# Kernel tuning notes

Measured on AMD Instinct MI355X. Metric: run time of the kernel, lower is better.

## Reference

```python
import jax, jax.numpy as jnp
import numpy as np

B, N, D = 2, 8192, 1024
H, Dh = 16, 64
P = H * Dh
EPS = 1e-6
DECAY_BIAS_SHIFT = 2.0


def setup_inputs() -> dict:
    key = jax.random.key(0)
    ks = jax.random.split(key, 7)
    s_in = 1.0 / np.sqrt(D)
    s_out = 1.0 / np.sqrt(P)
    return {
        "x": jax.random.normal(ks[0], (B, N, D), jnp.float32),
        "Wq": jax.random.normal(ks[1], (D, P), jnp.float32) * s_in,
        "Wk": jax.random.normal(ks[2], (D, P), jnp.float32) * s_in,
        "Wv": jax.random.normal(ks[3], (D, P), jnp.float32) * s_in,
        "Wo": jax.random.normal(ks[4], (P, D), jnp.float32) * s_out,
        "Wa": jax.random.normal(ks[5], (D, H), jnp.float32) * s_in,
        "ba": jnp.zeros((H,), jnp.float32),
    }


def _elu_plus_one(x):
    return jax.nn.elu(x) + 1.0


def _ssd_scan(q, k, v, a, eps):
    # q,k,v: (B,H,N,Dh); a: (B,H,N) in (0,1)
    # Recurrence: S_t = a_t*S_{t-1} + k_t v_t^T ; z_t = a_t*z_{t-1} + k_t
    # out_t = (q_t @ S_t) / (q_t . z_t + eps)
    qT = jnp.moveaxis(q, 2, 0)  # (N,B,H,Dh)
    kT = jnp.moveaxis(k, 2, 0)
    vT = jnp.moveaxis(v, 2, 0)
    aT = jnp.moveaxis(a, 2, 0)  # (N,B,H)

    Bb, Hh, _, Dk = q.shape
    Dv = v.shape[-1]
    S0 = jnp.zeros((Bb, Hh, Dk, Dv), q.dtype)
    z0 = jnp.zeros((Bb, Hh, Dk), q.dtype)

    def step(carry, inp):
        S, z = carry
        qt, kt, vt, at = inp
        S = at[..., None, None] * S + kt[..., :, None] * vt[..., None, :]
        z = at[..., None] * z + kt
        num = jnp.einsum("bhk,bhkv->bhv", qt, S)
        den = jnp.einsum("bhk,bhk->bh", qt, z) + eps
        return (S, z), num / den[..., None]

    _, outT = jax.lax.scan(step, (S0, z0), (qT, kT, vT, aT))
    return jnp.moveaxis(outT, 0, 2)  # (B,H,N,Dv)


def reference(x, Wq, Wk, Wv, Wo, Wa, ba):
    b, n, _ = x.shape
    q = (x @ Wq).reshape(b, n, H, Dh).transpose(0, 2, 1, 3)
    k = (x @ Wk).reshape(b, n, H, Dh).transpose(0, 2, 1, 3)
    v = (x @ Wv).reshape(b, n, H, Dh).transpose(0, 2, 1, 3)
    q = _elu_plus_one(q)
    k = _elu_plus_one(k)
    a = jax.nn.sigmoid(x @ Wa + ba + DECAY_BIAS_SHIFT)  # (B,N,H)
    a = a.transpose(0, 2, 1)  # (B,H,N)
    out = _ssd_scan(q, k, v, a, EPS)  # (B,H,N,Dh)
    out = out.transpose(0, 2, 1, 3).reshape(b, n, P)
    return out @ Wo
```

## Files before the change

kernel.cpp:

```cpp
#include <hip/hip_runtime.h>
#include <stdint.h>

#define HH 16
#define DH 64
#define DD 1024
#define PP 1024
#define NNLEN 8192
#define BBATCH 2
#define MM (BBATCH*NNLEN)
#define CCHUNK 128
#define LCH 64
#define NGRP 16
#define GCH 8
#define EPSV 1e-6f

typedef unsigned short u16;
typedef __attribute__((ext_vector_type(4))) unsigned short u16x4;
typedef __attribute__((ext_vector_type(8))) unsigned short u16x8;
typedef __attribute__((ext_vector_type(8))) __bf16 bf16x8;
typedef __attribute__((ext_vector_type(4))) float f32x4;

__device__ __forceinline__ u16 f2bf(float f) {
  unsigned x = __float_as_uint(f);
  return (u16)((x + 0x7fffu + ((x >> 16) & 1u)) >> 16);
}
__device__ __forceinline__ float bf2f(u16 u) {
  return __uint_as_float(((unsigned)u) << 16);
}

__device__ __forceinline__ void gl2lds16(const void* g, void* l) {
  __builtin_amdgcn_global_load_lds(
      reinterpret_cast<__attribute__((address_space(1))) void*>(
          reinterpret_cast<uintptr_t>(g)),
      reinterpret_cast<__attribute__((address_space(3))) void*>(
          reinterpret_cast<uintptr_t>(l)),
      16, 0, 0);
}

__device__ __forceinline__ bf16x8 ldsw(const u16* base, int row, int col) {
  union { u16x8 u; bf16x8 b; } cv;
  cv.u = *(const u16x8*)&base[row * 64 + (col ^ ((row & 7) << 3))];
  return cv.b;
}

__global__ __launch_bounds__(256)
void prep_all(const float* __restrict__ x, u16* __restrict__ xb,
              const float* __restrict__ Wq, u16* __restrict__ WqT,
              const float* __restrict__ Wk, u16* __restrict__ WkT,
              const float* __restrict__ Wv, u16* __restrict__ WvT,
              const float* __restrict__ Wo, u16* __restrict__ WoT,
              const float* __restrict__ Wa, u16* __restrict__ WaT) {
  __shared__ float tile[32][33];
  const int bid = blockIdx.x;
  const int tid = threadIdx.x;
  if (bid < 8192) {
    size_t i = ((size_t)bid * 256 + tid) * 8;
    f32x4 a = *(const f32x4*)(x + i);
    f32x4 b = *(const f32x4*)(x + i + 4);
    u16x8 o;
    o[0] = f2bf(a[0]); o[1] = f2bf(a[1]); o[2] = f2bf(a[2]); o[3] = f2bf(a[3]);
    o[4] = f2bf(b[0]); o[5] = f2bf(b[1]); o[6] = f2bf(b[2]); o[7] = f2bf(b[3]);
    *(u16x8*)(xb + i) = o;
    return;
  }
  if (bid < 12288) {
    const int t = (bid - 8192) >> 10;
    const int sub = (bid - 8192) & 1023;
    const float* in = (t == 0) ? Wq : (t == 1) ? Wk : (t == 2) ? Wv : Wo;
    u16* out = (t == 0) ? WqT : (t == 1) ? WkT : (t == 2) ? WvT : WoT;
    const int bx = (sub & 31) * 32, by = (sub >> 5) * 32;
    const int tx = tid & 31, ty = tid >> 5;
    for (int i2 = ty; i2 < 32; i2 += 8)
      tile[i2][tx] = in[(size_t)(by + i2) * 1024 + bx + tx];
    __syncthreads();
    for (int i2 = ty; i2 < 32; i2 += 8)
      out[(size_t)(bx + i2) * 1024 + by + tx] = f2bf(tile[tx][i2]);
    return;
  }
  {
    int idx = (bid - 12288) * 256 + tid;
    WaT[idx] = f2bf(Wa[(idx & 1023) * 16 + (idx >> 10)]);
  }
}

__global__ __launch_bounds__(256)
void a_proj(const u16* __restrict__ xb, const u16* __restrict__ WaT,
            const float* __restrict__ ba, float* __restrict__ abuf) {
  __shared__ __align__(16) u16 As[256 * 32];
  __shared__ __align__(16) u16 Bs[16 * 32];
  const int tid = threadIdx.x;
  const int brow = blockIdx.x * 256;
  const int l = tid & 63, wid = tid >> 6;
  const int la = l & 15, kb8 = (l >> 4) * 8;
  const int sr = tid >> 2, se = (tid & 3) * 8;

  f32x4 acc[4];
#pragma unroll
  for (int mi = 0; mi < 4; ++mi) acc[mi] = (f32x4){0.f, 0.f, 0.f, 0.f};

  for (int kt = 0; kt < 32; ++kt) {
    const int k0 = kt * 32;
    __syncthreads();
#pragma unroll
    for (int i = 0; i < 4; ++i)
      gl2lds16(xb + (size_t)(brow + i * 64 + sr) * DD + k0 + se,
               &As[i * 2048 + wid * 512]);
    if (wid == 0)
      gl2lds16(WaT + (size_t)(l >> 2) * DD + k0 + (l & 3) * 8, &Bs[0]);
    __syncthreads();
    union { u16x8 u; bf16x8 b; } cvb;
    cvb.u = *(const u16x8*)&Bs[la * 32 + kb8];
#pragma unroll
    for (int mi = 0; mi < 4; ++mi) {
      union { u16x8 u; bf16x8 b; } cva;
      cva.u = *(const u16x8*)&As[(wid * 64 + mi * 16 + la) * 32 + kb8];
      acc[mi] = __builtin_amdgcn_mfma_f32_16x16x32_bf16(cva.b, cvb.b, acc[mi], 0, 0, 0);
    }
  }
  const float bav = ba[la];
#pragma unroll
  for (int mi = 0; mi < 4; ++mi)
#pragma unroll
    for (int rr = 0; rr < 4; ++rr) {
      int row = brow + wid * 64 + mi * 16 + ((l >> 4) << 2) + rr;
      float t = acc[mi][rr] + bav + 2.0f;
      abuf[(size_t)row * HH + la] = 1.f / (1.f + __expf(-t));
    }
}

template<int NCT>
__global__ __launch_bounds__(1024, 4)
void gemm16(const u16* __restrict__ A, const u16* __restrict__ Bt,
            void* __restrict__ Cout) {
  __shared__ __align__(16) u16 As[2][256 * 64];
  __shared__ __align__(16) u16 Bs[2][256 * 64];
  const int tid = threadIdx.x;
  const int nwg = gridDim.x;
  const int f = blockIdx.x;
  const int swz = (f & 7) * (nwg >> 3) + (f >> 3);
  const int brow = (swz / NCT) * 256;
  const int bcol = (swz % NCT) * 256;
  const int l = tid & 63;
  const int wid = tid >> 6;
  const int wr = wid >> 2;
  const int wc = wid & 3;
  const int la = l & 15, kb8 = (l >> 4) * 8;
  const int K = 1024;
  const int srow = l >> 3;
  const int scol = ((l & 7) * 8) ^ (srow << 3);
  const int ldso = (wid * 2) * 512;

  f32x4 acc[4][4];
#pragma unroll
  for (int i = 0; i < 4; ++i)
#pragma unroll
    for (int j = 0; j < 4; ++j) acc[i][j] = (f32x4){0.f, 0.f, 0.f, 0.f};

#pragma unroll
  for (int j = 0; j < 2; ++j) {
    const int r0 = (wid * 2 + j) * 8 + srow;
    gl2lds16(A  + (size_t)(brow + r0) * K + scol, &As[0][ldso + j * 512]);
    gl2lds16(Bt + (size_t)(bcol + r0) * K + scol, &Bs[0][ldso + j * 512]);
  }
  asm volatile("s_waitcnt vmcnt(0)" ::: "memory");
  __builtin_amdgcn_s_barrier();

  const int NKT = K / 64;
  for (int kt = 0; kt < NKT; ++kt) {
    const u16* lA = As[kt & 1];
    const u16* lB = Bs[kt & 1];
    u16* nA = As[(kt + 1) & 1];
    u16* nB = Bs[(kt + 1) & 1];
    const int knext = (kt + 1) * 64;
    const bool more = (kt + 1 < NKT);

    if (more) {
#pragma unroll
      for (int j = 0; j < 2; ++j) {
        const int r0 = (wid * 2 + j) * 8 + srow;
        gl2lds16(A  + (size_t)(brow + r0) * K + knext + scol,
                 nA + ldso + j * 512);
        gl2lds16(Bt + (size_t)(bcol + r0) * K + knext + scol,
                 nB + ldso + j * 512);
      }
    }

    bf16x8 bfr[4][2];
#pragma unroll
    for (int n2 = 0; n2 < 4; ++n2)
#pragma unroll
      for (int kk = 0; kk < 2; ++kk)
        bfr[n2][kk] = ldsw(lB, wc * 64 + n2 * 16 + la, kk * 32 + kb8);

#pragma unroll
    for (int m2 = 0; m2 < 4; ++m2) {
      bf16x8 af0 = ldsw(lA, wr * 64 + m2 * 16 + la, kb8);
      bf16x8 af1 = ldsw(lA, wr * 64 + m2 * 16 + la, 32 + kb8);
      __builtin_amdgcn_s_setprio(1);
#pragma unroll
      for (int n2 = 0; n2 < 4; ++n2) {
        acc[m2][n2] = __builtin_amdgcn_mfma_f32_16x16x32_bf16(
            af0, bfr[n2][0], acc[m2][n2], 0, 0, 0);
        acc[m2][n2] = __builtin_amdgcn_mfma_f32_16x16x32_bf16(
            af1, bfr[n2][1], acc[m2][n2], 0, 0, 0);
      }
      __builtin_amdgcn_s_setprio(0);
    }

    if (more) {
      asm volatile("s_waitcnt vmcnt(0)" ::: "memory");
      __builtin_amdgcn_s_barrier();
    }
  }

  const int wrow = wr * 64, wcol = wc * 64;
  u16* base = (u16*)Cout + (size_t)(bcol >> 10) * ((size_t)MM * 1024);
  const bool act = (bcol < 2048);
#pragma unroll
  for (int mi = 0; mi < 4; ++mi)
#pragma unroll
    for (int ni = 0; ni < 4; ++ni)
#pragma unroll
      for (int rr = 0; rr < 4; ++rr) {
        int row = brow + wrow + mi * 16 + ((l >> 4) << 2) + rr;
        int c2 = (bcol & 1023) + wcol + ni * 16 + la;
        float v = acc[mi][ni][rr];
        if (act) v = v > 0.f ? v + 1.f : __expf(v);
        base[(size_t)row * 1024 + c2] = f2bf(v);
      }
}

template<int NCT>
__global__ __launch_bounds__(512)
void gemm_db(const u16* __restrict__ A, const u16* __restrict__ Bt,
             float* __restrict__ Cout) {
  __shared__ __align__(16) u16 As[2][256 * 64];
  __shared__ __align__(16) u16 Bs[2][256 * 64];
  const int tid = threadIdx.x;
  const int nwg = gridDim.x;
  const int f = blockIdx.x;
  const int swz = (f & 7) * (nwg >> 3) + (f >> 3);
  const int brow = (swz / NCT) * 256;
  const int bcol = (swz % NCT) * 256;
  const int l = tid & 63;
  const int wid = tid >> 6;
  const int wr = wid >> 2;
  const int wc = wid & 3;
  const int la = l & 15, kb8 = (l >> 4) * 8;
  const int K = 1024;
  const int srow = l >> 3;
  const int scol = ((l & 7) * 8) ^ (srow << 3);
  const int ldso = (wid * 2) * 512;

  f32x4 acc[8][4];
#pragma unroll
  for (int i = 0; i < 8; ++i)
#pragma unroll
    for (int j = 0; j < 4; ++j) acc[i][j] = (f32x4){0.f, 0.f, 0.f, 0.f};

#pragma unroll
  for (int h = 0; h < 2; ++h)
#pragma unroll
    for (int j = 0; j < 2; ++j) {
      const int r0 = h * 128 + (wid * 2 + j) * 8 + srow;
      gl2lds16(A  + (size_t)(brow + r0) * K + scol, &As[0][h * 8192 + ldso + j * 512]);
      gl2lds16(Bt + (size_t)(bcol + r0) * K + scol, &Bs[0][h * 8192 + ldso + j * 512]);
    }
  asm volatile("s_waitcnt vmcnt(0)" ::: "memory");
  __builtin_amdgcn_s_barrier();

  const int NKT = K / 64;
  for (int kt = 0; kt < NKT; ++kt) {
    const u16* lA = As[kt & 1];
    const u16* lB = Bs[kt & 1];
    u16* nA = As[(kt + 1) & 1];
    u16* nB = Bs[(kt + 1) & 1];
    const int knext = (kt + 1) * 64;
    const bool more = (kt + 1 < NKT);

    if (more) {
#pragma unroll
      for (int h = 0; h < 2; ++h)
#pragma unroll
        for (int j = 0; j < 2; ++j) {
          const int r0 = h * 128 + (wid * 2 + j) * 8 + srow;
          gl2lds16(A  + (size_t)(brow + r0) * K + knext + scol,
                   nA + h * 8192 + ldso + j * 512);
          gl2lds16(Bt + (size_t)(bcol + r0) * K + knext + scol,
                   nB + h * 8192 + ldso + j * 512);
        }
    }

    bf16x8 af[4][2], bfr[4][2];
#pragma unroll
    for (int m2 = 0; m2 < 4; ++m2)
#pragma unroll
      for (int kk = 0; kk < 2; ++kk)
        af[m2][kk] = ldsw(lA, wr * 128 + m2 * 16 + la, kk * 32 + kb8);
#pragma unroll
    for (int n2 = 0; n2 < 4; ++n2)
#pragma unroll
      for (int kk = 0; kk < 2; ++kk)
        bfr[n2][kk] = ldsw(lB, wc * 64 + n2 * 16 + la, kk * 32 + kb8);

    __builtin_amdgcn_s_setprio(1);
#pragma unroll
    for (int m2 = 0; m2 < 4; ++m2)
#pragma unroll
      for (int n2 = 0; n2 < 4; ++n2)
#pragma unroll
        for (int kk = 0; kk < 2; ++kk)
          acc[m2][n2] = __builtin_amdgcn_mfma_f32_16x16x32_bf16(
              af[m2][kk], bfr[n2][kk], acc[m2][n2], 0, 0, 0);
    __builtin_amdgcn_s_setprio(0);

#pragma unroll
    for (int m2 = 0; m2 < 4; ++m2)
#pragma unroll
      for (int kk = 0; kk < 2; ++kk)
        af[m2][kk] = ldsw(lA, wr * 128 + 64 + m2 * 16 + la, kk * 32 + kb8);

    __builtin_amdgcn_s_setprio(1);
#pragma unroll
    for (int m2 = 0; m2 < 4; ++m2)
#pragma unroll
      for (int n2 = 0; n2 < 4; ++n2)
#pragma unroll
        for (int kk = 0; kk < 2; ++kk)
          acc[4 + m2][n2] = __builtin_amdgcn_mfma_f32_16x16x32_bf16(
              af[m2][kk], bfr[n2][kk], acc[4 + m2][n2], 0, 0, 0);
    __builtin_amdgcn_s_setprio(0);

    if (more) {
      asm volatile("s_waitcnt vmcnt(0)" ::: "memory");
      __builtin_amdgcn_s_barrier();
    }
  }

  const int wrow = wr * 128, wcol = wc * 64;
#pragma unroll
  for (int mi = 0; mi < 8; ++mi)
#pragma unroll
    for (int ni = 0; ni < 4; ++ni)
#pragma unroll
      for (int rr = 0; rr < 4; ++rr) {
        int row = brow + wrow + mi * 16 + ((l >> 4) << 2) + rr;
        int col = bcol + wcol + ni * 16 + la;
        Cout[(size_t)row * 1024 + col] = acc[mi][ni][rr];
      }
}

__global__ __launch_bounds__(256)
void chunk_local_scan(const u16* __restrict__ kb, const u16* __restrict__ vb,
                      const float* __restrict__ abuf,
                      u16* __restrict__ Sbuf, float* __restrict__ zbuf,
                      float* __restrict__ cAbuf,
                      float* __restrict__ GAgg, float* __restrict__ zGAgg,
                      float* __restrict__ dpbuf) {
  const int g = blockIdx.x & (NGRP - 1);
  const int bh = blockIdx.x >> 4;
  const int h = bh & (HH - 1);
  const int b = bh >> 4;
  __shared__ __align__(16) u16 KT[64 * 64];
  __shared__ __align__(16) u16 VTl[64 * 64];
  __shared__ float wshA[GCH][64];
  __shared__ float dchA[GCH];
  const int tid = threadIdx.x;
  const int r = tid >> 2, e = (tid & 3) * 16;
  const int l = tid & 63, w = tid >> 6;
  const int kb8 = (l >> 4) << 3, la = l & 15;
  const int dw = 16 * w + ((l >> 4) << 2);
  const int dkz = tid >> 2, tqz = (tid & 3) * 16, swkz = (dkz & 7) << 3;
  const int c0 = g * GCH;
  const int rowbase0 = b * NNLEN + c0 * LCH;

#pragma unroll
  for (int ii = 0; ii < 2; ++ii) {
    const int i = w * 2 + ii;
    const int blkc = bh * CCHUNK + c0 + i;
    float v = __logf(abuf[(size_t)(rowbase0 + i * LCH + l) * HH + h]);
#pragma unroll
    for (int d = 1; d < 64; d <<= 1) {
      float u = __shfl_up(v, d);
      if (l >= d) v += u;
    }
    cAbuf[(size_t)blkc * 64 + l] = v;
    float tot = __shfl(v, 63);
    wshA[i][l] = __expf(tot - v);
    if (l == 0) dchA[i] = __expf(tot);
  }
  __syncthreads();
  if (tid == 0) {
    float rp = 1.f;
#pragma unroll
    for (int i = 0; i < GCH; ++i) {
      dpbuf[bh * CCHUNK + c0 + i] = rp;
      rp *= dchA[i];
    }
  }

  f32x4 run[4];
#pragma unroll
  for (int ni = 0; ni < 4; ++ni) run[ni] = (f32x4){0.f, 0.f, 0.f, 0.f};
  float zrun = 0.f;

  const u16* kp = kb + (size_t)(rowbase0 + r) * PP + h * DH + e;
  const u16* vp = vb + (size_t)(rowbase0 + r) * PP + h * DH + e;
  u16x8 k0 = *(const u16x8*)kp, k1 = *(const u16x8*)(kp + 8);
  u16x8 v0 = *(const u16x8*)vp, v1 = *(const u16x8*)(vp + 8);

  for (int i = 0; i < GCH; ++i) {
    const int blkc = bh * CCHUNK + c0 + i;
    if (i) __syncthreads();

    {
      const float wt = wshA[i][r];
#pragma unroll
      for (int j = 0; j < 8; ++j) {
        int d0 = e + j, d1 = e + 8 + j;
        KT[d0 * 64 + (r ^ ((d0 & 7) << 3))] = f2bf(bf2f(k0[j]) * wt);
        KT[d1 * 64 + (r ^ ((d1 & 7) << 3))] = f2bf(bf2f(k1[j]) * wt);
        VTl[d0 * 64 + (r ^ ((d0 & 7) << 3))] = v0[j];
        VTl[d1 * 64 + (r ^ ((d1 & 7) << 3))] = v1[j];
      }
    }
    __syncthreads();

    if (i + 1 < GCH) {
      const int rb = rowbase0 + (i + 1) * LCH;
      kp = kb + (size_t)(rb + r) * PP + h * DH + e;
      vp = vb + (size_t)(rb + r) * PP + h * DH + e;
      k0 = *(const u16x8*)kp; k1 = *(const u16x8*)(kp + 8);
      v0 = *(const u16x8*)vp; v1 = *(const u16x8*)(vp + 8);
    }

    const float dch = dchA[i];
    f32x4 s[4];
#pragma unroll
    for (int ni = 0; ni < 4; ++ni) s[ni] = (f32x4){0.f, 0.f, 0.f, 0.f};
#pragma unroll
    for (int kk = 0; kk < 2; ++kk) {
      bf16x8 av = ldsw(VTl, 16 * w + la, kk * 32 + kb8);
#pragma unroll
      for (int ni = 0; ni < 4; ++ni)
        s[ni] = __builtin_amdgcn_mfma_f32_16x16x32_bf16(
            av, ldsw(KT, 16 * ni + la, kk * 32 + kb8), s[ni], 0, 0, 0);
    }

    u16* Sc = Sbuf + (size_t)blkc * 4096;
#pragma unroll
    for (int ni = 0; ni < 4; ++ni)
#pragma unroll
      for (int rr = 0; rr < 4; ++rr)
        Sc[(dw + rr) * 64 + 16 * ni + la] = f2bf(run[ni][rr]);
#pragma unroll
    for (int ni = 0; ni < 4; ++ni)
#pragma unroll
      for (int rr = 0; rr < 4; ++rr)
        run[ni][rr] = dch * run[ni][rr] + s[ni][rr];

    {
      float zp = 0.f;
#pragma unroll
      for (int i2 = 0; i2 < 16; ++i2)
        zp += bf2f(KT[dkz * 64 + ((tqz + i2) ^ swkz)]);
      zp += __shfl_xor(zp, 1);
      zp += __shfl_xor(zp, 2);
      if ((tid & 3) == 0) zbuf[(size_t)blkc * 64 + dkz] = zrun;
      zrun = dch * zrun + zp;
    }
  }

  float* Ga = GAgg + ((size_t)bh * NGRP + g) * 4096;
#pragma unroll
  for (int ni = 0; ni < 4; ++ni)
#pragma unroll
    for (int rr = 0; rr < 4; ++rr)
      Ga[(dw + rr) * 64 + 16 * ni + la] = run[ni][rr];
  if ((tid & 3) == 0)
    zGAgg[((size_t)bh * NGRP + g) * 64 + dkz] = zrun;
}

__global__ __launch_bounds__(1024)
void scan_top(const float* __restrict__ GAgg, u16* __restrict__ GBeg,
              float* __restrict__ zGAgg, const float* __restrict__ cAbuf) {
  const int bh = blockIdx.x;
  const size_t cb = (size_t)bh * CCHUNK;
  __shared__ float Dsh[NGRP];
  if (threadIdx.x < NGRP) {
    float s = 0.f;
#pragma unroll
    for (int i = 0; i < GCH; ++i)
      s += cAbuf[(cb + threadIdx.x * GCH + i) * 64 + 63];
    Dsh[threadIdx.x] = __expf(s);
  }
  __syncthreads();
  const int elem = threadIdx.x * 4;
  const float* base = GAgg + (size_t)bh * NGRP * 4096;
  u16* gb = GBeg + (size_t)bh * NGRP * 4096;
  f32x4 run = (f32x4){0.f, 0.f, 0.f, 0.f};
  f32x4 cur = *(const f32x4*)&base[elem];
#pragma unroll
  for (int gg = 0; gg < NGRP; ++gg) {
    f32x4 nxt;
    if (gg + 1 < NGRP) nxt = *(const f32x4*)&base[(gg + 1) * 4096 + elem];
    u16x4 o;
#pragma unroll
    for (int jj = 0; jj < 4; ++jj) o[jj] = f2bf(run[jj]);
    *(u16x4*)&gb[gg * 4096 + elem] = o;
    const float D = Dsh[gg];
#pragma unroll
    for (int jj = 0; jj < 4; ++jj) run[jj] = D * run[jj] + cur[jj];
    cur = nxt;
  }
  if (threadIdx.x < 64) {
    float* zb = zGAgg + (size_t)bh * NGRP * 64;
    float zr = 0.f;
#pragma unroll
    for (int gg = 0; gg < NGRP; ++gg) {
      float a = zb[gg * 64 + threadIdx.x];
      zb[gg * 64 + threadIdx.x] = zr;
      zr = Dsh[gg] * zr + a;
    }
  }
}

__global__ __launch_bounds__(256)
void chunk_out(u16* __restrict__ qb, const u16* __restrict__ kb,
               const u16* __restrict__ vb, const u16* __restrict__ Sbuf,
               const float* __restrict__ zbuf, const float* __restrict__ cAbuf,
               const u16* __restrict__ GBeg, const float* __restrict__ zGAgg,
               const float* __restrict__ dpbuf) {
  const int blk = blockIdx.x;
  const int c = blk & (CCHUNK - 1);
  const int h = (blk >> 7) & (HH - 1);
  const int b = blk >> 11;
  const int bh = blk >> 7;
  const int g = c >> 3;
  const int rowbase = b * NNLEN + c * LCH;

  __shared__ __align__(16) u16 Qs[64 * 64];
  __shared__ __align__(16) u16 Ke[64 * 64];
  __shared__ __align__(16) u16 VT[64 * 64];
  __shared__ __align__(16) u16 STs[64 * 64];
  __shared__ float cAsh[64], zsh[64], denP[64], qzs[64];

  const int tid = threadIdx.x;
  const int r = tid >> 2, e = (tid & 3) * 16;
  const float dp = dpbuf[blk];

  const u16* qp = qb + (size_t)(rowbase + r) * PP + h * DH + e;
  const u16* kp = kb + (size_t)(rowbase + r) * PP + h * DH + e;
  const u16* vp = vb + (size_t)(rowbase + r) * PP + h * DH + e;
  u16x8 q0 = *(const u16x8*)qp, q1 = *(const u16x8*)(qp + 8);
  u16x8 k0 = *(const u16x8*)kp, k1 = *(const u16x8*)(kp + 8);
  u16x8 v0 = *(const u16x8*)vp, v1 = *(const u16x8*)(vp + 8);
  const u16* sp = Sbuf + (size_t)blk * 4096 + r * 64 + e;
  u16x8 p0 = *(const u16x8*)sp, p1 = *(const u16x8*)(sp + 8);
  const u16* gp = GBeg + ((size_t)bh * NGRP + g) * 4096 + r * 64 + e;
  u16x8 gb0 = *(const u16x8*)gp, gb1 = *(const u16x8*)(gp + 8);
  if (tid < 64) {
    cAsh[tid] = cAbuf[(size_t)blk * 64 + tid];
    zsh[tid] = zbuf[(size_t)blk * 64 + tid]
             + dp * zGAgg[((size_t)bh * NGRP + g) * 64 + tid];
  }
  __syncthreads();

  {
    const float c0c = cAsh[31];
    const int sw = (r & 7) << 3;
    const float qsc = __expf(cAsh[r] - c0c);
    const float ksc = __expf(c0c - cAsh[r]);
    const float ssc = __expf(c0c);
    u16x8 t0, t1, u0, u1, w0, w1;
#pragma unroll
    for (int j = 0; j < 8; ++j) {
      t0[j] = f2bf(bf2f(q0[j]) * qsc);
      t1[j] = f2bf(bf2f(q1[j]) * qsc);
      u0[j] = f2bf(bf2f(k0[j]) * ksc);
      u1[j] = f2bf(bf2f(k1[j]) * ksc);
    }
#pragma unroll
    for (int j = 0; j < 8; ++j) {
      w0[j] = f2bf((bf2f(p0[j]) + dp * bf2f(gb0[j])) * ssc);
      w1[j] = f2bf((bf2f(p1[j]) + dp * bf2f(gb1[j])) * ssc);
    }
    *(u16x8*)&Qs[r * 64 + (e ^ sw)] = t0;
    *(u16x8*)&Qs[r * 64 + ((e + 8) ^ sw)] = t1;
    *(u16x8*)&Ke[r * 64 + (e ^ sw)] = u0;
    *(u16x8*)&Ke[r * 64 + ((e + 8) ^ sw)] = u1;
    *(u16x8*)&STs[r * 64 + (e ^ sw)] = w0;
    *(u16x8*)&STs[r * 64 + ((e + 8) ^ sw)] = w1;
#pragma unroll
    for (int j = 0; j < 8; ++j) {
      int d0 = e + j, d1 = e + 8 + j;
      VT[d0 * 64 + (r ^ ((d0 & 7) << 3))] = v0[j];
      VT[d1 * 64 + (r ^ ((d1 & 7) << 3))] = v1[j];
    }
    if (tid < 64) zsh[tid] *= ssc;
  }
  __syncthreads();

  const int l = tid & 63, w = tid >> 6;
  const int kb8 = (l >> 4) << 3, la = l & 15;

  bf16x8 aq[2];
  f32x4 p[4];
#pragma unroll
  for (int ni = 0; ni < 4; ++ni) p[ni] = (f32x4){0.f, 0.f, 0.f, 0.f};
#pragma unroll
  for (int kk = 0; kk < 2; ++kk) {
    aq[kk] = ldsw(Qs, 16 * w + la, kk * 32 + kb8);
#pragma unroll
    for (int ni = 0; ni < 4; ++ni)
      p[ni] = __builtin_amdgcn_mfma_f32_16x16x32_bf16(
          aq[kk], ldsw(Ke, 16 * ni + la, kk * 32 + kb8), p[ni], 0, 0, 0);
  }

  const int tw = 16 * w + ((l >> 4) << 2);
  float rsum[4] = {0.f, 0.f, 0.f, 0.f};
#pragma unroll
  for (int ni = 0; ni < 4; ++ni)
#pragma unroll
    for (int rr = 0; rr < 4; ++rr) {
      int s = 16 * ni + la, t = tw + rr;
      float v = (s <= t) ? p[ni][rr] : 0.f;
      p[ni][rr] = v;
      rsum[rr] += v;
    }
#pragma unroll
  for (int d = 1; d < 16; d <<= 1)
#pragma unroll
    for (int rr = 0; rr < 4; ++rr) rsum[rr] += __shfl_xor(rsum[rr], d);
  if (la == 0)
#pragma unroll
    for (int rr = 0; rr < 4; ++rr) denP[tw + rr] = rsum[rr];

  {
    float qzp = 0.f;
#pragma unroll
    for (int kk = 0; kk < 2; ++kk)
#pragma unroll
      for (int j = 0; j < 8; ++j) {
        union { bf16x8 b; u16x8 u; } cv; cv.b = aq[kk];
        qzp += bf2f(cv.u[j]) * zsh[kk * 32 + kb8 + j];
      }
    qzp += __shfl_xor(qzp, 16);
    qzp += __shfl_xor(qzp, 32);
    if (l < 16) qzs[16 * w + la] = qzp;
  }
  __syncthreads();

#pragma unroll
  for (int ni = 0; ni < 4; ++ni)
#pragma unroll
    for (int rr = 0; rr < 4; ++rr) {
      int t = tw + rr, s = 16 * ni + la;
      Ke[t * 64 + (s ^ ((t & 7) << 3))] = f2bf(p[ni][rr]);
    }
  __syncthreads();

  f32x4 o[4];
#pragma unroll
  for (int ni = 0; ni < 4; ++ni) o[ni] = (f32x4){0.f, 0.f, 0.f, 0.f};
#pragma unroll
  for (int kk = 0; kk < 2; ++kk) {
    bf16x8 ap = ldsw(Ke, 16 * w + la, kk * 32 + kb8);
#pragma unroll
    for (int ni = 0; ni < 4; ++ni)
      o[ni] = __builtin_amdgcn_mfma_f32_16x16x32_bf16(
          ap, ldsw(VT, 16 * ni + la, kk * 32 + kb8), o[ni], 0, 0, 0);
  }
#pragma unroll
  for (int kk = 0; kk < 2; ++kk)
#pragma unroll
    for (int ni = 0; ni < 4; ++ni)
      o[ni] = __builtin_amdgcn_mfma_f32_16x16x32_bf16(
          aq[kk], ldsw(STs, 16 * ni + la, kk * 32 + kb8), o[ni], 0, 0, 0);

  float dn[4];
#pragma unroll
  for (int rr = 0; rr < 4; ++rr) dn[rr] = qzs[tw + rr] + denP[tw + rr] + EPSV;
#pragma unroll
  for (int ni = 0; ni < 4; ++ni)
#pragma unroll
    for (int rr = 0; rr < 4; ++rr) {
      int t = tw + rr, dv = 16 * ni + la;
      qb[(size_t)(rowbase + t) * PP + h * DH + dv] = f2bf(o[ni][rr] / dn[rr]);
    }
}

extern "C" void kernel_launch(void* const* d_in, const int* in_sizes, int n_in,
                              void* d_out, int out_size, void* d_ws, size_t ws_size,
                              hipStream_t stream) {
  const float* x  = (const float*)d_in[0];
  const float* Wq = (const float*)d_in[1];
  const float* Wk = (const float*)d_in[2];
  const float* Wv = (const float*)d_in[3];
  const float* Wo = (const float*)d_in[4];
  const float* Wa = (const float*)d_in[5];
  const float* ba = (const float*)d_in[6];

  char* ws = (char*)d_ws;
  size_t off = 0;
  auto carve = [&](size_t bytes) {
    void* p = ws + off;
    off += (bytes + 255) & ~(size_t)255;
    return p;
  };
  u16* xb   = (u16*)carve((size_t)MM * DD * 2);
  u16* WqT  = (u16*)carve((size_t)PP * DD * 2);
  u16* WkT  = (u16*)carve((size_t)PP * DD * 2);
  u16* WvT  = (u16*)carve((size_t)PP * DD * 2);
  u16* WoT  = (u16*)carve((size_t)DD * PP * 2);
  u16* WaT  = (u16*)carve((size_t)HH * DD * 2);
  u16* qb   = (u16*)carve((size_t)MM * PP * 2);
  u16* kb   = (u16*)carve((size_t)MM * PP * 2);
  u16* vb   = (u16*)carve((size_t)MM * PP * 2);
  float* abuf  = (float*)carve((size_t)MM * HH * 4);
  u16*  Sbuf   = (u16*)carve((size_t)BBATCH * HH * CCHUNK * 4096 * 2);
  float* zbuf  = (float*)carve((size_t)BBATCH * HH * CCHUNK * 64 * 4);
  float* cAbuf = (float*)carve((size_t)BBATCH * HH * CCHUNK * 64 * 4);
  float* GAgg  = (float*)carve((size_t)BBATCH * HH * NGRP * 4096 * 4);
  u16*  GBeg   = (u16*)carve((size_t)BBATCH * HH * NGRP * 4096 * 2);
  float* zGAgg = (float*)carve((size_t)BBATCH * HH * NGRP * 64 * 4);
  float* dpbuf = (float*)carve((size_t)BBATCH * HH * CCHUNK * 4);

  prep_all<<<12352, 256, 0, stream>>>(x, xb, Wq, WqT, Wk, WkT, Wv, WvT,
                                      Wo, WoT, Wa, WaT);
  a_proj<<<MM / 256, 256, 0, stream>>>(xb, WaT, ba, abuf);

  gemm16<12><<<(MM / 256) * 12, 1024, 0, stream>>>(xb, WqT, qb);

  chunk_local_scan<<<BBATCH * HH * NGRP, 256, 0, stream>>>(
      kb, vb, abuf, Sbuf, zbuf, cAbuf, GAgg, zGAgg, dpbuf);
  scan_top<<<BBATCH * HH, 1024, 0, stream>>>(GAgg, GBeg, zGAgg, cAbuf);
  chunk_out<<<BBATCH * HH * CCHUNK, 256, 0, stream>>>(qb, kb, vb, Sbuf, zbuf, cAbuf,
                                                      GBeg, zGAgg, dpbuf);

  gemm_db<4><<<(MM / 256) * 4, 512, 0, stream>>>(qb, WoT, (float*)d_out);
}
```

Baseline: 254.2 us.

## Double-buffer a_proj loads and shrink its row tile for more blocks

Result: faster. 243.8 us, median of 3 (-4.1%).

```diff
diff --git a/kernel.cpp b/kernel.cpp
--- a/kernel.cpp
+++ b/kernel.cpp
@@ -86,46 +86,48 @@
 __global__ __launch_bounds__(256)
 void a_proj(const u16* __restrict__ xb, const u16* __restrict__ WaT,
             const float* __restrict__ ba, float* __restrict__ abuf) {
-  __shared__ __align__(16) u16 As[256 * 32];
-  __shared__ __align__(16) u16 Bs[16 * 32];
+  __shared__ __align__(16) u16 As[2][64 * 32];
+  __shared__ __align__(16) u16 Bs[2][16 * 32];
   const int tid = threadIdx.x;
-  const int brow = blockIdx.x * 256;
+  const int brow = blockIdx.x * 64;
   const int l = tid & 63, wid = tid >> 6;
   const int la = l & 15, kb8 = (l >> 4) * 8;
   const int sr = tid >> 2, se = (tid & 3) * 8;
 
-  f32x4 acc[4];
-#pragma unroll
-  for (int mi = 0; mi < 4; ++mi) acc[mi] = (f32x4){0.f, 0.f, 0.f, 0.f};
+  f32x4 acc = (f32x4){0.f, 0.f, 0.f, 0.f};
+
+  gl2lds16(xb + (size_t)(brow + sr) * DD + se, &As[0][wid * 512]);
+  if (wid == 0)
+    gl2lds16(WaT + (size_t)(l >> 2) * DD + (l & 3) * 8, &Bs[0][0]);
+  asm volatile("s_waitcnt vmcnt(0)" ::: "memory");
+  __builtin_amdgcn_s_barrier();
 
   for (int kt = 0; kt < 32; ++kt) {
-    const int k0 = kt * 32;
-    __syncthreads();
-#pragma unroll
-    for (int i = 0; i < 4; ++i)
-      gl2lds16(xb + (size_t)(brow + i * 64 + sr) * DD + k0 + se,
-               &As[i * 2048 + wid * 512]);
-    if (wid == 0)
-      gl2lds16(WaT + (size_t)(l >> 2) * DD + k0 + (l & 3) * 8, &Bs[0]);
-    __syncthreads();
-    union { u16x8 u; bf16x8 b; } cvb;
-    cvb.u = *(const u16x8*)&Bs[la * 32 + kb8];
-#pragma unroll
-    for (int mi = 0; mi < 4; ++mi) {
-      union { u16x8 u; bf16x8 b; } cva;
-      cva.u = *(const u16x8*)&As[(wid * 64 + mi * 16 + la) * 32 + kb8];
-      acc[mi] = __builtin_amdgcn_mfma_f32_16x16x32_bf16(cva.b, cvb.b, acc[mi], 0, 0, 0);
+    const bool more = (kt + 1 < 32);
+    if (more) {
+      const int kn = (kt + 1) * 32;
+      gl2lds16(xb + (size_t)(brow + sr) * DD + kn + se,
+               &As[(kt + 1) & 1][wid * 512]);
+      if (wid == 0)
+        gl2lds16(WaT + (size_t)(l >> 2) * DD + kn + (l & 3) * 8,
+                 &Bs[(kt + 1) & 1][0]);
+    }
+    union { u16x8 u; bf16x8 b; } cva, cvb;
+    cvb.u = *(const u16x8*)&Bs[kt & 1][la * 32 + kb8];
+    cva.u = *(const u16x8*)&As[kt & 1][(wid * 16 + la) * 32 + kb8];
+    acc = __builtin_amdgcn_mfma_f32_16x16x32_bf16(cva.b, cvb.b, acc, 0, 0, 0);
+    if (more) {
+      asm volatile("s_waitcnt vmcnt(0)" ::: "memory");
+      __builtin_amdgcn_s_barrier();
     }
   }
   const float bav = ba[la];
 #pragma unroll
-  for (int mi = 0; mi < 4; ++mi)
-#pragma unroll
-    for (int rr = 0; rr < 4; ++rr) {
-      int row = brow + wid * 64 + mi * 16 + ((l >> 4) << 2) + rr;
-      float t = acc[mi][rr] + bav + 2.0f;
-      abuf[(size_t)row * HH + la] = 1.f / (1.f + __expf(-t));
-    }
+  for (int rr = 0; rr < 4; ++rr) {
+    int row = brow + wid * 16 + ((l >> 4) << 2) + rr;
+    float t = acc[rr] + bav + 2.0f;
+    abuf[(size_t)row * HH + la] = 1.f / (1.f + __expf(-t));
+  }
 }
 
 template<int NCT>
@@ -728,7 +730,7 @@
 
   prep_all<<<12352, 256, 0, stream>>>(x, xb, Wq, WqT, Wk, WkT, Wv, WvT,
                                       Wo, WoT, Wa, WaT);
-  a_proj<<<MM / 256, 256, 0, stream>>>(xb, WaT, ba, abuf);
+  a_proj<<<MM / 64, 256, 0, stream>>>(xb, WaT, ba, abuf);
 
   gemm16<12><<<(MM / 256) * 12, 1024, 0, stream>>>(xb, WqT, qb);
 
```

## Fuse decay projection into x conversion and load chunk_out operands directly into MFMA registers

Applied to the files above, without the earlier changes.

Result: slower. 290.2 us (+14.2%).

```diff
diff --git a/kernel.cpp b/kernel.cpp
--- a/kernel.cpp
+++ b/kernel.cpp
@@ -49,23 +49,50 @@
               const float* __restrict__ Wk, u16* __restrict__ WkT,
               const float* __restrict__ Wv, u16* __restrict__ WvT,
               const float* __restrict__ Wo, u16* __restrict__ WoT,
-              const float* __restrict__ Wa, u16* __restrict__ WaT) {
-  __shared__ float tile[32][33];
+              const float* __restrict__ Wa, const float* __restrict__ ba,
+              float* __restrict__ abuf) {
   const int bid = blockIdx.x;
   const int tid = threadIdx.x;
-  if (bid < 8192) {
-    size_t i = ((size_t)bid * 256 + tid) * 8;
-    f32x4 a = *(const f32x4*)(x + i);
-    f32x4 b = *(const f32x4*)(x + i + 4);
-    u16x8 o;
-    o[0] = f2bf(a[0]); o[1] = f2bf(a[1]); o[2] = f2bf(a[2]); o[3] = f2bf(a[3]);
-    o[4] = f2bf(b[0]); o[5] = f2bf(b[1]); o[6] = f2bf(b[2]); o[7] = f2bf(b[3]);
-    *(u16x8*)(xb + i) = o;
+  if (bid < 256) {
+    __shared__ __align__(16) u16 As[64 * 40];
+    const int brow = bid * 64;
+    const int row = tid >> 2, col8 = (tid & 3) * 8;
+    const int l = tid & 63, wid = tid >> 6;
+    const int la = l & 15, kb8 = (l >> 4) * 8;
+    f32x4 acc = (f32x4){0.f, 0.f, 0.f, 0.f};
+    for (int kt = 0; kt < 32; ++kt) {
+      const int k0 = kt * 32;
+      const float* xr = x + (size_t)(brow + row) * DD + k0 + col8;
+      f32x4 a = *(const f32x4*)xr;
+      f32x4 b2 = *(const f32x4*)(xr + 4);
+      u16x8 o;
+      o[0] = f2bf(a[0]);  o[1] = f2bf(a[1]);  o[2] = f2bf(a[2]);  o[3] = f2bf(a[3]);
+      o[4] = f2bf(b2[0]); o[5] = f2bf(b2[1]); o[6] = f2bf(b2[2]); o[7] = f2bf(b2[3]);
+      *(u16x8*)(xb + (size_t)(brow + row) * DD + k0 + col8) = o;
+      if (kt) __syncthreads();
+      *(u16x8*)&As[row * 40 + col8] = o;
+      __syncthreads();
+      union { u16x8 u; bf16x8 b; } cvb, cva;
+#pragma unroll
+      for (int j = 0; j < 8; ++j)
+        cvb.u[j] = f2bf(Wa[(size_t)(k0 + kb8 + j) * HH + la]);
+      cva.u = *(const u16x8*)&As[(wid * 16 + la) * 40 + kb8];
+      acc = __builtin_amdgcn_mfma_f32_16x16x32_bf16(cva.b, cvb.b, acc, 0, 0, 0);
+    }
+    const float bav = ba[la];
+#pragma unroll
+    for (int rr = 0; rr < 4; ++rr) {
+      int row2 = brow + wid * 16 + ((l >> 4) << 2) + rr;
+      float t = acc[rr] + bav + 2.0f;
+      abuf[(size_t)row2 * HH + la] = 1.f / (1.f + __expf(-t));
+    }
     return;
   }
-  if (bid < 12288) {
-    const int t = (bid - 8192) >> 10;
-    const int sub = (bid - 8192) & 1023;
+  {
+    __shared__ float tile[32][33];
+    const int bid2 = bid - 256;
+    const int t = bid2 >> 10;
+    const int sub = bid2 & 1023;
     const float* in = (t == 0) ? Wq : (t == 1) ? Wk : (t == 2) ? Wv : Wo;
     u16* out = (t == 0) ? WqT : (t == 1) ? WkT : (t == 2) ? WvT : WoT;
     const int bx = (sub & 31) * 32, by = (sub >> 5) * 32;
@@ -75,57 +102,7 @@
     __syncthreads();
     for (int i2 = ty; i2 < 32; i2 += 8)
       out[(size_t)(bx + i2) * 1024 + by + tx] = f2bf(tile[tx][i2]);
-    return;
-  }
-  {
-    int idx = (bid - 12288) * 256 + tid;
-    WaT[idx] = f2bf(Wa[(idx & 1023) * 16 + (idx >> 10)]);
-  }
-}
-
-__global__ __launch_bounds__(256)
-void a_proj(const u16* __restrict__ xb, const u16* __restrict__ WaT,
-            const float* __restrict__ ba, float* __restrict__ abuf) {
-  __shared__ __align__(16) u16 As[256 * 32];
-  __shared__ __align__(16) u16 Bs[16 * 32];
-  const int tid = threadIdx.x;
-  const int brow = blockIdx.x * 256;
-  const int l = tid & 63, wid = tid >> 6;
-  const int la = l & 15, kb8 = (l >> 4) * 8;
-  const int sr = tid >> 2, se = (tid & 3) * 8;
-
-  f32x4 acc[4];
-#pragma unroll
-  for (int mi = 0; mi < 4; ++mi) acc[mi] = (f32x4){0.f, 0.f, 0.f, 0.f};
-
-  for (int kt = 0; kt < 32; ++kt) {
-    const int k0 = kt * 32;
-    __syncthreads();
-#pragma unroll
-    for (int i = 0; i < 4; ++i)
-      gl2lds16(xb + (size_t)(brow + i * 64 + sr) * DD + k0 + se,
-               &As[i * 2048 + wid * 512]);
-    if (wid == 0)
-      gl2lds16(WaT + (size_t)(l >> 2) * DD + k0 + (l & 3) * 8, &Bs[0]);
-    __syncthreads();
-    union { u16x8 u; bf16x8 b; } cvb;
-    cvb.u = *(const u16x8*)&Bs[la * 32 + kb8];
-#pragma unroll
-    for (int mi = 0; mi < 4; ++mi) {
-      union { u16x8 u; bf16x8 b; } cva;
-      cva.u = *(const u16x8*)&As[(wid * 64 + mi * 16 + la) * 32 + kb8];
-      acc[mi] = __builtin_amdgcn_mfma_f32_16x16x32_bf16(cva.b, cvb.b, acc[mi], 0, 0, 0);
-    }
-  }
-  const float bav = ba[la];
-#pragma unroll
-  for (int mi = 0; mi < 4; ++mi)
-#pragma unroll
-    for (int rr = 0; rr < 4; ++rr) {
-      int row = brow + wid * 64 + mi * 16 + ((l >> 4) << 2) + rr;
-      float t = acc[mi][rr] + bav + 2.0f;
-      abuf[(size_t)row * HH + la] = 1.f / (1.f + __expf(-t));
-    }
+  }
 }
 
 template<int NCT>
@@ -539,85 +516,67 @@
   const int g = c >> 3;
   const int rowbase = b * NNLEN + c * LCH;
 
-  __shared__ __align__(16) u16 Qs[64 * 64];
-  __shared__ __align__(16) u16 Ke[64 * 64];
   __shared__ __align__(16) u16 VT[64 * 64];
-  __shared__ __align__(16) u16 STs[64 * 64];
-  __shared__ float cAsh[64], zsh[64], denP[64], qzs[64];
+  __shared__ __align__(16) u16 Pb[64 * 64];
+  __shared__ float cAsh[64], zsh[64], qzs[64];
 
   const int tid = threadIdx.x;
   const int r = tid >> 2, e = (tid & 3) * 16;
   const float dp = dpbuf[blk];
 
-  const u16* qp = qb + (size_t)(rowbase + r) * PP + h * DH + e;
-  const u16* kp = kb + (size_t)(rowbase + r) * PP + h * DH + e;
   const u16* vp = vb + (size_t)(rowbase + r) * PP + h * DH + e;
-  u16x8 q0 = *(const u16x8*)qp, q1 = *(const u16x8*)(qp + 8);
-  u16x8 k0 = *(const u16x8*)kp, k1 = *(const u16x8*)(kp + 8);
   u16x8 v0 = *(const u16x8*)vp, v1 = *(const u16x8*)(vp + 8);
-  const u16* sp = Sbuf + (size_t)blk * 4096 + r * 64 + e;
-  u16x8 p0 = *(const u16x8*)sp, p1 = *(const u16x8*)(sp + 8);
-  const u16* gp = GBeg + ((size_t)bh * NGRP + g) * 4096 + r * 64 + e;
-  u16x8 gb0 = *(const u16x8*)gp, gb1 = *(const u16x8*)(gp + 8);
   if (tid < 64) {
-    cAsh[tid] = cAbuf[(size_t)blk * 64 + tid];
-    zsh[tid] = zbuf[(size_t)blk * 64 + tid]
-             + dp * zGAgg[((size_t)bh * NGRP + g) * 64 + tid];
-  }
-  __syncthreads();
-
-  {
-    const float c0c = cAsh[31];
-    const int sw = (r & 7) << 3;
-    const float qsc = __expf(cAsh[r] - c0c);
-    const float ksc = __expf(c0c - cAsh[r]);
-    const float ssc = __expf(c0c);
-    u16x8 t0, t1, u0, u1, w0, w1;
-#pragma unroll
-    for (int j = 0; j < 8; ++j) {
-      t0[j] = f2bf(bf2f(q0[j]) * qsc);
-      t1[j] = f2bf(bf2f(q1[j]) * qsc);
-      u0[j] = f2bf(bf2f(k0[j]) * ksc);
-      u1[j] = f2bf(bf2f(k1[j]) * ksc);
-    }
-#pragma unroll
-    for (int j = 0; j < 8; ++j) {
-      w0[j] = f2bf((bf2f(p0[j]) + dp * bf2f(gb0[j])) * ssc);
-      w1[j] = f2bf((bf2f(p1[j]) + dp * bf2f(gb1[j])) * ssc);
-    }
-    *(u16x8*)&Qs[r * 64 + (e ^ sw)] = t0;
-    *(u16x8*)&Qs[r * 64 + ((e + 8) ^ sw)] = t1;
-    *(u16x8*)&Ke[r * 64 + (e ^ sw)] = u0;
-    *(u16x8*)&Ke[r * 64 + ((e + 8) ^ sw)] = u1;
-    *(u16x8*)&STs[r * 64 + (e ^ sw)] = w0;
-    *(u16x8*)&STs[r * 64 + ((e + 8) ^ sw)] = w1;
-#pragma unroll
-    for (int j = 0; j < 8; ++j) {
-      int d0 = e + j, d1 = e + 8 + j;
-      VT[d0 * 64 + (r ^ ((d0 & 7) << 3))] = v0[j];
-      VT[d1 * 64 + (r ^ ((d1 & 7) << 3))] = v1[j];
-    }
-    if (tid < 64) zsh[tid] *= ssc;
+    float ca = cAbuf[(size_t)blk * 64 + tid];
+    cAsh[tid] = ca;
+    float c0 = cAbuf[(size_t)blk * 64 + 31];
+    zsh[tid] = (zbuf[(size_t)blk * 64 + tid]
+              + dp * zGAgg[((size_t)bh * NGRP + g) * 64 + tid]) * __expf(c0);
+  }
+#pragma unroll
+  for (int j = 0; j < 8; ++j) {
+    int d0 = e + j, d1 = e + 8 + j;
+    VT[d0 * 64 + (r ^ ((d0 & 7) << 3))] = v0[j];
+    VT[d1 * 64 + (r ^ ((d1 & 7) << 3))] = v1[j];
   }
   __syncthreads();
 
   const int l = tid & 63, w = tid >> 6;
   const int kb8 = (l >> 4) << 3, la = l & 15;
+  const int tw = 16 * w + ((l >> 4) << 2);
+  const float c0c = cAsh[31];
 
   bf16x8 aq[2];
+  {
+    const float qsc = __expf(cAsh[16 * w + la] - c0c);
+    const u16* qp = qb + (size_t)(rowbase + 16 * w + la) * PP + h * DH;
+#pragma unroll
+    for (int kk = 0; kk < 2; ++kk) {
+      u16x8 q8 = *(const u16x8*)(qp + kk * 32 + kb8);
+      union { u16x8 u; bf16x8 b; } cv;
+#pragma unroll
+      for (int j = 0; j < 8; ++j) cv.u[j] = f2bf(bf2f(q8[j]) * qsc);
+      aq[kk] = cv.b;
+    }
+  }
+
   f32x4 p[4];
 #pragma unroll
   for (int ni = 0; ni < 4; ++ni) p[ni] = (f32x4){0.f, 0.f, 0.f, 0.f};
 #pragma unroll
-  for (int kk = 0; kk < 2; ++kk) {
-    aq[kk] = ldsw(Qs, 16 * w + la, kk * 32 + kb8);
-#pragma unroll
-    for (int ni = 0; ni < 4; ++ni)
-      p[ni] = __builtin_amdgcn_mfma_f32_16x16x32_bf16(
-          aq[kk], ldsw(Ke, 16 * ni + la, kk * 32 + kb8), p[ni], 0, 0, 0);
-  }
-
-  const int tw = 16 * w + ((l >> 4) << 2);
+  for (int ni = 0; ni < 4; ++ni) {
+    const float ksc = __expf(c0c - cAsh[16 * ni + la]);
+    const u16* kp = kb + (size_t)(rowbase + 16 * ni + la) * PP + h * DH;
+#pragma unroll
+    for (int kk = 0; kk < 2; ++kk) {
+      u16x8 k8 = *(const u16x8*)(kp + kk * 32 + kb8);
+      union { u16x8 u; bf16x8 b; } cv;
+#pragma unroll
+      for (int j = 0; j < 8; ++j) cv.u[j] = f2bf(bf2f(k8[j]) * ksc);
+      p[ni] = __builtin_amdgcn_mfma_f32_16x16x32_bf16(aq[kk], cv.b, p[ni], 0, 0, 0);
+    }
+  }
+
   float rsum[4] = {0.f, 0.f, 0.f, 0.f};
 #pragma unroll
   for (int ni = 0; ni < 4; ++ni)
@@ -632,55 +591,62 @@
   for (int d = 1; d < 16; d <<= 1)
 #pragma unroll
     for (int rr = 0; rr < 4; ++rr) rsum[rr] += __shfl_xor(rsum[rr], d);
-  if (la == 0)
-#pragma unroll
-    for (int rr = 0; rr < 4; ++rr) denP[tw + rr] = rsum[rr];
 
   {
     float qzp = 0.f;
 #pragma unroll
-    for (int kk = 0; kk < 2; ++kk)
-#pragma unroll
-      for (int j = 0; j < 8; ++j) {
-        union { bf16x8 b; u16x8 u; } cv; cv.b = aq[kk];
+    for (int kk = 0; kk < 2; ++kk) {
+      union { bf16x8 b; u16x8 u; } cv; cv.b = aq[kk];
+#pragma unroll
+      for (int j = 0; j < 8; ++j)
         qzp += bf2f(cv.u[j]) * zsh[kk * 32 + kb8 + j];
-      }
+    }
     qzp += __shfl_xor(qzp, 16);
     qzp += __shfl_xor(qzp, 32);
     if (l < 16) qzs[16 * w + la] = qzp;
   }
-  __syncthreads();
 
 #pragma unroll
   for (int ni = 0; ni < 4; ++ni)
 #pragma unroll
     for (int rr = 0; rr < 4; ++rr) {
       int t = tw + rr, s = 16 * ni + la;
-      Ke[t * 64 + (s ^ ((t & 7) << 3))] = f2bf(p[ni][rr]);
-    }
-  __syncthreads();
+      Pb[t * 64 + (s ^ ((t & 7) << 3))] = f2bf(p[ni][rr]);
+    }
 
   f32x4 o[4];
 #pragma unroll
   for (int ni = 0; ni < 4; ++ni) o[ni] = (f32x4){0.f, 0.f, 0.f, 0.f};
 #pragma unroll
   for (int kk = 0; kk < 2; ++kk) {
-    bf16x8 ap = ldsw(Ke, 16 * w + la, kk * 32 + kb8);
+    bf16x8 ap = ldsw(Pb, 16 * w + la, kk * 32 + kb8);
 #pragma unroll
     for (int ni = 0; ni < 4; ++ni)
       o[ni] = __builtin_amdgcn_mfma_f32_16x16x32_bf16(
           ap, ldsw(VT, 16 * ni + la, kk * 32 + kb8), o[ni], 0, 0, 0);
   }
-#pragma unroll
-  for (int kk = 0; kk < 2; ++kk)
-#pragma unroll
-    for (int ni = 0; ni < 4; ++ni)
-      o[ni] = __builtin_amdgcn_mfma_f32_16x16x32_bf16(
-          aq[kk], ldsw(STs, 16 * ni + la, kk * 32 + kb8), o[ni], 0, 0, 0);
+  {
+    const float ssc = __expf(c0c);
+#pragma unroll
+    for (int ni = 0; ni < 4; ++ni) {
+      const u16* sp = Sbuf + (size_t)blk * 4096 + (16 * ni + la) * 64;
+      const u16* gp = GBeg + ((size_t)bh * NGRP + g) * 4096 + (16 * ni + la) * 64;
+#pragma unroll
+      for (int kk = 0; kk < 2; ++kk) {
+        u16x8 s8 = *(const u16x8*)(sp + kk * 32 + kb8);
+        u16x8 g8 = *(const u16x8*)(gp + kk * 32 + kb8);
+        union { u16x8 u; bf16x8 b; } cv;
+#pragma unroll
+        for (int j = 0; j < 8; ++j)
+          cv.u[j] = f2bf((bf2f(s8[j]) + dp * bf2f(g8[j])) * ssc);
+        o[ni] = __builtin_amdgcn_mfma_f32_16x16x32_bf16(aq[kk], cv.b, o[ni], 0, 0, 0);
+      }
+    }
+  }
 
   float dn[4];
 #pragma unroll
-  for (int rr = 0; rr < 4; ++rr) dn[rr] = qzs[tw + rr] + denP[tw + rr] + EPSV;
+  for (int rr = 0; rr < 4; ++rr) dn[rr] = qzs[tw + rr] + rsum[rr] + EPSV;
 #pragma unroll
   for (int ni = 0; ni < 4; ++ni)
 #pragma unroll
@@ -713,7 +679,6 @@
   u16* WkT  = (u16*)carve((size_t)PP * DD * 2);
   u16* WvT  = (u16*)carve((size_t)PP * DD * 2);
   u16* WoT  = (u16*)carve((size_t)DD * PP * 2);
-  u16* WaT  = (u16*)carve((size_t)HH * DD * 2);
   u16* qb   = (u16*)carve((size_t)MM * PP * 2);
   u16* kb   = (u16*)carve((size_t)MM * PP * 2);
   u16* vb   = (u16*)carve((size_t)MM * PP * 2);
@@ -726,9 +691,8 @@
   float* zGAgg = (float*)carve((size_t)BBATCH * HH * NGRP * 64 * 4);
   float* dpbuf = (float*)carve((size_t)BBATCH * HH * CCHUNK * 4);
 
-  prep_all<<<12352, 256, 0, stream>>>(x, xb, Wq, WqT, Wk, WkT, Wv, WvT,
-                                      Wo, WoT, Wa, WaT);
-  a_proj<<<MM / 256, 256, 0, stream>>>(xb, WaT, ba, abuf);
+  prep_all<<<4352, 256, 0, stream>>>(x, xb, Wq, WqT, Wk, WkT, Wv, WvT,
+                                     Wo, WoT, Wa, ba, abuf);
 
   gemm16<12><<<(MM / 256) * 12, 1024, 0, stream>>>(xb, WqT, qb);
 
```
